# Kernel tuning notes

Measured on AMD Instinct MI355X. Metric: run time of the kernel, lower is better.

## Reference

```python
import jax, jax.numpy as jnp
import numpy as np

B, S, D, H, E = 4, 2048, 1024, 2048, 8
TOP_K = 2


def setup_inputs() -> dict:
    key = jax.random.key(0)
    ks = jax.random.split(key, 6)
    s = 0.02
    x = jax.random.normal(ks[0], (B, S, D), dtype=jnp.float32)
    # torch nn.Linear stores weight as [out_features, in_features]
    W1 = jax.random.normal(ks[1], (E, H, D), dtype=jnp.float32) * s  # dim -> hidden
    W2 = jax.random.normal(ks[2], (E, D, H), dtype=jnp.float32) * s  # hidden -> dim
    W3 = jax.random.normal(ks[3], (E, H, D), dtype=jnp.float32) * s  # dim -> hidden
    gate_w = jax.random.normal(ks[4], (E, D), dtype=jnp.float32) * s
    gate_b = jnp.zeros((E,), dtype=jnp.float32)
    return {"x": x, "W1": W1, "W2": W2, "W3": W3, "gate_w": gate_w, "gate_b": gate_b}


def reference(x, W1, W2, W3, gate_w, gate_b):
    b, s, d = x.shape
    xf = x.reshape(-1, d)                                  # [N, D], N = B*S
    logits = xf @ gate_w.T + gate_b                        # [N, E]
    probs = jax.nn.softmax(logits, axis=-1)
    top2_p, top2_i = jax.lax.top_k(probs, TOP_K)           # [N, 2]
    top2_p = top2_p / jnp.sum(top2_p, axis=-1, keepdims=True)
    out = jnp.zeros_like(xf)
    n_experts = W1.shape[0]
    for e in range(n_experts):  # small fixed expert loop
        # combine weight for tokens routed to expert e (0 if not routed)
        coef = jnp.sum(jnp.where(top2_i == e, top2_p, 0.0), axis=-1)  # [N]
        h = jnp.maximum(xf @ W1[e].T, 0.0) ** 2 * (xf @ W3[e].T)      # relu(x)^2 * x  [N, H]
        out = out + coef[:, None] * (h @ W2[e].T)                     # [N, D]
    return out.reshape(b, s, d)
```

## Files before the change

### kernel.cpp

```cpp
#include <hip/hip_runtime.h>
#include <hip/hip_fp16.h>
#include <math.h>

#define N_TOK 8192
#define D_DIM 1024
#define H_DIM 2048
#define N_EXP 8
#define CAPL  8192
#define MT1   18

typedef _Float16 f16x8 __attribute__((ext_vector_type(8)));
typedef float    f32x4 __attribute__((ext_vector_type(4)));

__device__ __forceinline__ void gload16(const void* g, void* l) {
  __builtin_amdgcn_global_load_lds(
      (const __attribute__((address_space(1))) void*)g,
      (__attribute__((address_space(3))) void*)l, 16, 0, 0);
}

__global__ __launch_bounds__(256) void cvt_f32_f16(const float* __restrict__ s,
                                                   _Float16* __restrict__ d, int n4) {
  int i = blockIdx.x * 256 + threadIdx.x;
  if (i >= n4) return;
  float4 v = ((const float4*)s)[i];
  _Float16 o0 = (_Float16)v.x, o1 = (_Float16)v.y, o2 = (_Float16)v.z, o3 = (_Float16)v.w;
  __attribute__((ext_vector_type(4))) _Float16 o = {o0, o1, o2, o3};
  ((__attribute__((ext_vector_type(4))) _Float16*)d)[i] = o;
}

__global__ __launch_bounds__(256) void pack_w(const float* __restrict__ src,
                                              _Float16* __restrict__ dst,
                                              int R, int K) {
  const int e = blockIdx.z, rt = blockIdx.y, kc = blockIdx.x;
  const int t = threadIdx.x;
  const int r = t >> 1, c = (t & 1) * 16;
  const float* s = src + ((long)e * R + (long)rt * 128 + r) * K + kc * 32 + c;
  const float4 v0 = ((const float4*)s)[0];
  const float4 v1 = ((const float4*)s)[1];
  const float4 v2 = ((const float4*)s)[2];
  const float4 v3 = ((const float4*)s)[3];
  f16x8 o0, o1;
  o0[0]=(_Float16)v0.x; o0[1]=(_Float16)v0.y; o0[2]=(_Float16)v0.z; o0[3]=(_Float16)v0.w;
  o0[4]=(_Float16)v1.x; o0[5]=(_Float16)v1.y; o0[6]=(_Float16)v1.z; o0[7]=(_Float16)v1.w;
  o1[0]=(_Float16)v2.x; o1[1]=(_Float16)v2.y; o1[2]=(_Float16)v2.z; o1[3]=(_Float16)v2.w;
  o1[4]=(_Float16)v3.x; o1[5]=(_Float16)v3.y; o1[6]=(_Float16)v3.z; o1[7]=(_Float16)v3.w;
  _Float16* d = dst + (((long)e * (R >> 7) + rt) * (K >> 5) + kc) * 4096 + t * 16;
  ((f16x8*)d)[0] = o0;
  ((f16x8*)d)[1] = o1;
}

__global__ __launch_bounds__(256) void gate_compute(
    const float* __restrict__ x, const float* __restrict__ gw,
    const float* __restrict__ gb, int* __restrict__ e12,
    float2* __restrict__ pp) {
  __shared__ float sgw[N_EXP * D_DIM];
  for (int i = threadIdx.x; i < N_EXP * D_DIM; i += 256) sgw[i] = gw[i];
  __syncthreads();
  const int w = threadIdx.x >> 6, lane = threadIdx.x & 63;
  const int n = blockIdx.x * 4 + w;
  const float* xp = x + (long)n * D_DIM;
  double acc[N_EXP];
  #pragma unroll
  for (int e = 0; e < N_EXP; e++) acc[e] = 0.0;
  for (int i = 0; i < D_DIM / 64; i++) {
    int d = lane + i * 64;
    double xv = (double)xp[d];
    #pragma unroll
    for (int e = 0; e < N_EXP; e++) acc[e] += xv * (double)sgw[e * D_DIM + d];
  }
  #pragma unroll
  for (int e = 0; e < N_EXP; e++)
    for (int off = 32; off >= 1; off >>= 1)
      acc[e] += __shfl_down(acc[e], off);
  if (lane == 0) {
    double lg[N_EXP];
    #pragma unroll
    for (int e = 0; e < N_EXP; e++) lg[e] = acc[e] + (double)gb[e];
    int i1 = 0;
    for (int e = 1; e < N_EXP; e++) if (lg[e] > lg[i1]) i1 = e;
    int i2 = (i1 == 0) ? 1 : 0;
    for (int e = 0; e < N_EXP; e++) { if (e == i1) continue; if (lg[e] > lg[i2]) i2 = e; }
    double p1 = 1.0 / (1.0 + exp(lg[i2] - lg[i1]));
    double p2 = 1.0 - p1;
    e12[n] = i1 | (i2 << 8);
    pp[n] = make_float2((float)p1, (float)p2);
  }
}

__global__ __launch_bounds__(256) void build_lists(
    const int* __restrict__ e12, const float2* __restrict__ pp,
    int* __restrict__ cnt, int* __restrict__ tokL, float* __restrict__ coefL) {
  const int e = blockIdx.x;
  __shared__ int sbase;
  __shared__ int wsum[4];
  const int w = threadIdx.x >> 6, lane = threadIdx.x & 63;
  if (threadIdx.x == 0) sbase = 0;
  __syncthreads();
  for (int c0 = 0; c0 < N_TOK; c0 += 256) {
    const int n = c0 + threadIdx.x;
    const int v = e12[n];
    const float2 pv = pp[n];
    int slot = -1;
    float p = 0.f;
    if ((v & 255) == e)      { slot = 0; p = pv.x; }
    else if ((v >> 8) == e)  { slot = 1; p = pv.y; }
    const unsigned long long m = __ballot(slot >= 0);
    if (lane == 0) wsum[w] = __popcll(m);
    __syncthreads();
    int wbase = sbase;
    #pragma unroll
    for (int i = 0; i < 4; i++) if (i < w) wbase += wsum[i];
    const int total = wsum[0] + wsum[1] + wsum[2] + wsum[3];
    if (slot >= 0) {
      const int pos = wbase + __popcll(m & ((1ull << lane) - 1ull));
      tokL[e * CAPL + pos] = n * 2 + slot;
      coefL[e * CAPL + pos] = p;
    }
    __syncthreads();
    if (threadIdx.x == 0) sbase += total;
  }
  __syncthreads();
  if (threadIdx.x == 0) cnt[e] = sbase;
}

__global__ __launch_bounds__(384, 2) void ffn_stage1(
    const _Float16* __restrict__ xh, const _Float16* __restrict__ w1p,
    const _Float16* __restrict__ w3p, const int* __restrict__ cnt,
    const int* __restrict__ tokL, _Float16* __restrict__ hbuf) {
  const int lin = blockIdx.x;
  const int xcd = lin & 7;
  const int j   = lin >> 3;
  const int mt  = j % MT1;
  const int gi  = j / MT1;
  const int g   = gi * 8 + xcd;
  const int nt  = g & 15;
  const int e   = g >> 4;
  const int m0 = mt * 128;
  const int c = cnt[e];
  if (m0 >= c) return;

  __shared__ _Float16 Xs[2][4096];
  __shared__ _Float16 W1s[2][4096];
  __shared__ _Float16 W3s[2][4096];
  __shared__ int sEnt[128];

  const int t = threadIdx.x;
  if (t < 128) {
    int idx = m0 + t; if (idx >= c) idx = c - 1;
    sEnt[t] = tokL[e * CAPL + idx];
  }
  __syncthreads();

  if (t >= 256) {
    const int pt = t - 256;
    const int swz = ((pt & 3) ^ ((pt >> 3) & 3)) * 8;
    const _Float16* xsrc[4];
    #pragma unroll
    for (int j2 = 0; j2 < 4; j2++)
      xsrc[j2] = xh + (long)(sEnt[(pt >> 2) + 32 * j2] >> 1) * D_DIM + swz;
    const int po = (pt >> 2) * 32 + swz;
    const _Float16* w1t = w1p + (long)(e * 16 + nt) * 32 * 4096 + po;
    const _Float16* w3t = w3p + (long)(e * 16 + nt) * 32 * 4096 + po;
    const int l0 = pt * 8;

    auto stage = [&](int b, int kc) {
      #pragma unroll
      for (int j2 = 0; j2 < 4; j2++)
        gload16(xsrc[j2] + kc * 32, &Xs[b][l0 + j2 * 1024]);
      #pragma unroll
      for (int j2 = 0; j2 < 4; j2++)
        gload16(w1t + (long)kc * 4096 + j2 * 1024, &W1s[b][l0 + j2 * 1024]);
      #pragma unroll
      for (int j2 = 0; j2 < 4; j2++)
        gload16(w3t + (long)kc * 4096 + j2 * 1024, &W3s[b][l0 + j2 * 1024]);
    };

    stage(0, 0);
    __asm__ volatile("s_waitcnt vmcnt(0)\n\ts_barrier");
    for (int kc = 0; kc < 32; ++kc) {
      if (kc + 1 < 32) stage((kc + 1) & 1, kc + 1);
      __asm__ volatile("s_waitcnt vmcnt(0)\n\ts_barrier");
    }
    return;
  }

  const int w = t >> 6, lane = t & 63;
  const int wm = (w & 1) * 64, wn = (w >> 1) * 64;
  const int q = lane >> 4, lr = lane & 15;
  const int qs = (q ^ ((lr >> 1) & 3)) * 8;

  f32x4 au[4][4], av[4][4];
  const f32x4 zz = {0.f, 0.f, 0.f, 0.f};
  #pragma unroll
  for (int i = 0; i < 4; i++)
    #pragma unroll
    for (int j2 = 0; j2 < 4; j2++) { au[i][j2] = zz; av[i][j2] = zz; }

  __syncthreads();
  for (int kc = 0; kc < 32; ++kc) {
    const int p = kc & 1;
    f16x8 a[4], b1[4], b3[4];
    #pragma unroll
    for (int i = 0; i < 4; i++) {
      a[i]  = *(const f16x8*)(&Xs[p][(wm + i * 16 + lr) * 32 + qs]);
      b1[i] = *(const f16x8*)(&W1s[p][(wn + i * 16 + lr) * 32 + qs]);
      b3[i] = *(const f16x8*)(&W3s[p][(wn + i * 16 + lr) * 32 + qs]);
    }
    #pragma unroll
    for (int mi = 0; mi < 4; mi++)
      #pragma unroll
      for (int ni = 0; ni < 4; ni++) {
        au[mi][ni] = __builtin_amdgcn_mfma_f32_16x16x32_f16(a[mi], b1[ni], au[mi][ni], 0, 0, 0);
        av[mi][ni] = __builtin_amdgcn_mfma_f32_16x16x32_f16(a[mi], b3[ni], av[mi][ni], 0, 0, 0);
      }
    __syncthreads();
  }

  const long tb = ((long)(e * MT1 + mt) * 64 + nt * 4) * 4096;
  #pragma unroll
  for (int mi = 0; mi < 4; mi++) {
    #pragma unroll
    for (int r = 0; r < 4; r++) {
      int ml = wm + mi * 16 + q * 4 + r;
      if (m0 + ml < c) {
        #pragma unroll
        for (int ni = 0; ni < 4; ni++) {
          int colb = wn + ni * 16;
          float u = au[mi][ni][r];
          float rl = u > 0.f ? u : 0.f;
          float hv = rl * rl * av[mi][ni][r];
          hbuf[tb + (long)(colb >> 5) * 4096 + ml * 32 + (colb & 31) + lr] = (_Float16)hv;
        }
      }
    }
  }
}

__global__ __launch_bounds__(384, 3) void ffn_stage2(
    const _Float16* __restrict__ hbuf, const _Float16* __restrict__ w2p,
    const int* __restrict__ cnt, const int* __restrict__ tokL,
    const float* __restrict__ coefL, float* __restrict__ out) {
  const int lin = blockIdx.x;
  const int xcd = lin & 7;
  const int j   = lin >> 3;
  const int mt  = j % MT1;
  const int gi  = j / MT1;
  const int g   = gi * 8 + xcd;
  const int dt  = g & 7;
  const int ezk = g >> 3;
  const int e   = ezk >> 1, ks = ezk & 1;
  const int m0 = mt * 128;
  const int c = cnt[e];
  if (m0 >= c) return;

  __shared__ _Float16 Hs[3][4096];
  __shared__ _Float16 W2s[3][4096];
  __shared__ int sEnt[128];
  __shared__ float sCoef[128];

  const int t = threadIdx.x;
  if (t < 128) {
    int idx = m0 + t; if (idx >= c) idx = c - 1;
    sEnt[t]  = tokL[e * CAPL + idx];
    sCoef[t] = coefL[e * CAPL + idx];
  }
  __syncthreads();

  if (t >= 256) {
    const int pt = t - 256;
    const int swz = ((pt & 3) ^ ((pt >> 3) & 3)) * 8;
    const int po = (pt >> 2) * 32 + swz;
    const _Float16* hA  = hbuf + ((long)(e * MT1 + mt) * 64 + ks * 32) * 4096 + po;
    const _Float16* w2t = w2p  + ((long)(e * 8 + dt) * 64 + ks * 32) * 4096 + po;
    const int l0 = pt * 8;

    auto stage = [&](int b, int kc) {
      #pragma unroll
      for (int j2 = 0; j2 < 4; j2++)
        gload16(hA + (long)kc * 4096 + j2 * 1024, &Hs[b][l0 + j2 * 1024]);
      #pragma unroll
      for (int j2 = 0; j2 < 4; j2++)
        gload16(w2t + (long)kc * 4096 + j2 * 1024, &W2s[b][l0 + j2 * 1024]);
    };

    stage(0, 0); stage(1, 1);
    __asm__ volatile("s_waitcnt vmcnt(8)\n\ts_barrier");
    for (int kc = 0; kc < 32; ++kc) {
      if (kc + 2 < 32) {
        stage((kc + 2) % 3, kc + 2);
        __asm__ volatile("s_waitcnt vmcnt(8)\n\ts_barrier");
      } else {
        __asm__ volatile("s_waitcnt vmcnt(0)\n\ts_barrier");
      }
    }
    return;
  }

  const int w = t >> 6, lane = t & 63;
  const int wm = (w & 1) * 64, wn = (w >> 1) * 64;
  const int q = lane >> 4, lr = lane & 15;
  const int qs = (q ^ ((lr >> 1) & 3)) * 8;

  f32x4 ac[4][4];
  const f32x4 zz = {0.f, 0.f, 0.f, 0.f};
  #pragma unroll
  for (int i = 0; i < 4; i++)
    #pragma unroll
    for (int j2 = 0; j2 < 4; j2++) ac[i][j2] = zz;

  __syncthreads();
  for (int kc = 0; kc < 32; ++kc) {
    const int p = kc % 3;
    f16x8 a[4], b[4];
    #pragma unroll
    for (int i = 0; i < 4; i++) {
      a[i] = *(const f16x8*)(&Hs[p][(wm + i * 16 + lr) * 32 + qs]);
      b[i] = *(const f16x8*)(&W2s[p][(wn + i * 16 + lr) * 32 + qs]);
    }
    #pragma unroll
    for (int mi = 0; mi < 4; mi++)
      #pragma unroll
      for (int ni = 0; ni < 4; ni++)
        ac[mi][ni] = __builtin_amdgcn_mfma_f32_16x16x32_f16(a[mi], b[ni], ac[mi][ni], 0, 0, 0);
    __syncthreads();
  }

  const int n0 = dt * 128;
  #pragma unroll
  for (int mi = 0; mi < 4; mi++) {
    #pragma unroll
    for (int r = 0; r < 4; r++) {
      int ml = wm + mi * 16 + q * 4 + r;
      if (m0 + ml < c) {
        int token = sEnt[ml] >> 1;
        float cf = sCoef[ml];
        float* op = out + (long)token * D_DIM + n0 + wn + lr;
        #pragma unroll
        for (int ni = 0; ni < 4; ni++)
          atomicAdd(op + ni * 16, cf * ac[mi][ni][r]);
      }
    }
  }
}

extern "C" void kernel_launch(void* const* d_in, const int* in_sizes, int n_in,
                              void* d_out, int out_size, void* d_ws, size_t ws_size,
                              hipStream_t stream) {
  (void)in_sizes; (void)n_in; (void)out_size; (void)ws_size;
  const float* x  = (const float*)d_in[0];
  const float* W1 = (const float*)d_in[1];
  const float* W2 = (const float*)d_in[2];
  const float* W3 = (const float*)d_in[3];
  const float* gw = (const float*)d_in[4];
  const float* gb = (const float*)d_in[5];
  float* out = (float*)d_out;

  _Float16* xh  = (_Float16*)d_ws;
  _Float16* w1p = xh  + (size_t)N_TOK * D_DIM;
  _Float16* w3p = w1p + (size_t)N_EXP * H_DIM * D_DIM;
  _Float16* w2p = w3p + (size_t)N_EXP * H_DIM * D_DIM;
  _Float16* hb  = w2p + (size_t)N_EXP * H_DIM * D_DIM;
  int*   cnt   = (int*)(hb + (size_t)N_EXP * MT1 * 64 * 4096);
  int*   tokL  = cnt + 16;
  float* coefL = (float*)(tokL + N_EXP * CAPL);
  int*   e12   = (int*)(coefL + N_EXP * CAPL);
  float2* pp   = (float2*)(e12 + N_TOK);

  hipMemsetAsync(d_out, 0, (size_t)N_TOK * D_DIM * sizeof(float), stream);

  int xn4 = N_TOK * D_DIM / 4;
  cvt_f32_f16<<<(xn4 + 255) / 256, 256, 0, stream>>>(x, xh, xn4);
  pack_w<<<dim3(D_DIM / 32, H_DIM / 128, N_EXP), 256, 0, stream>>>(W1, w1p, H_DIM, D_DIM);
  pack_w<<<dim3(D_DIM / 32, H_DIM / 128, N_EXP), 256, 0, stream>>>(W3, w3p, H_DIM, D_DIM);
  pack_w<<<dim3(H_DIM / 32, D_DIM / 128, N_EXP), 256, 0, stream>>>(W2, w2p, D_DIM, H_DIM);

  gate_compute<<<N_TOK / 4, 256, 0, stream>>>(x, gw, gb, e12, pp);
  build_lists<<<N_EXP, 256, 0, stream>>>(e12, pp, cnt, tokL, coefL);

  ffn_stage1<<<MT1 * 16 * N_EXP, 384, 0, stream>>>(xh, w1p, w3p, cnt, tokL, hb);
  ffn_stage2<<<MT1 * 8 * N_EXP * 2, 384, 0, stream>>>(hb, w2p, cnt, tokL, coefL, out);
}
```

Measured before the change: 687.6 us.

## Drop producer-wave specialization; have compute waves issue their own LDS prefetches

Both FFN GEMM stages previously used 384-thread blocks, with one extra wave group acting only as an async global-to-LDS loader, synchronized with the compute waves through barriers. This removes the producer waves. The 256 compute threads now issue the next k-chunk's global_load_lds themselves at the top of each iteration, with double buffering, and stage 2 drops from triple to double buffering. The goal is to cut the extra waves and their barrier traffic, freeing registers, LDS and wave slots for higher occupancy. The cost is that the compute waves now carry the load issue and wait on the loads at each barrier, with only one stage of prefetch in flight.

```diff
diff --git a/kernel.cpp b/kernel.cpp
--- a/kernel.cpp
+++ b/kernel.cpp
@@ -123,7 +123,7 @@
   if (threadIdx.x == 0) cnt[e] = sbase;
 }
 
-__global__ __launch_bounds__(384, 2) void ffn_stage1(
+__global__ __launch_bounds__(256, 2) void ffn_stage1(
     const _Float16* __restrict__ xh, const _Float16* __restrict__ w1p,
     const _Float16* __restrict__ w3p, const int* __restrict__ cnt,
     const int* __restrict__ tokL, _Float16* __restrict__ hbuf) {
@@ -151,38 +151,22 @@
   }
   __syncthreads();
 
-  if (t >= 256) {
-    const int pt = t - 256;
-    const int swz = ((pt & 3) ^ ((pt >> 3) & 3)) * 8;
-    const _Float16* xsrc[4];
-    #pragma unroll
-    for (int j2 = 0; j2 < 4; j2++)
-      xsrc[j2] = xh + (long)(sEnt[(pt >> 2) + 32 * j2] >> 1) * D_DIM + swz;
-    const int po = (pt >> 2) * 32 + swz;
-    const _Float16* w1t = w1p + (long)(e * 16 + nt) * 32 * 4096 + po;
-    const _Float16* w3t = w3p + (long)(e * 16 + nt) * 32 * 4096 + po;
-    const int l0 = pt * 8;
-
-    auto stage = [&](int b, int kc) {
-      #pragma unroll
-      for (int j2 = 0; j2 < 4; j2++)
-        gload16(xsrc[j2] + kc * 32, &Xs[b][l0 + j2 * 1024]);
-      #pragma unroll
-      for (int j2 = 0; j2 < 4; j2++)
-        gload16(w1t + (long)kc * 4096 + j2 * 1024, &W1s[b][l0 + j2 * 1024]);
-      #pragma unroll
-      for (int j2 = 0; j2 < 4; j2++)
-        gload16(w3t + (long)kc * 4096 + j2 * 1024, &W3s[b][l0 + j2 * 1024]);
-    };
-
-    stage(0, 0);
-    __asm__ volatile("s_waitcnt vmcnt(0)\n\ts_barrier");
-    for (int kc = 0; kc < 32; ++kc) {
-      if (kc + 1 < 32) stage((kc + 1) & 1, kc + 1);
-      __asm__ volatile("s_waitcnt vmcnt(0)\n\ts_barrier");
-    }
-    return;
-  }
+  const int swz = ((t & 3) ^ ((t >> 3) & 3)) * 8;
+  const _Float16* xsrcA = xh + (long)(sEnt[t >> 2] >> 1) * D_DIM + swz;
+  const _Float16* xsrcB = xh + (long)(sEnt[(t >> 2) + 64] >> 1) * D_DIM + swz;
+  const int po = (t >> 2) * 32 + swz;
+  const _Float16* w1t = w1p + (long)(e * 16 + nt) * 32 * 4096 + po;
+  const _Float16* w3t = w3p + (long)(e * 16 + nt) * 32 * 4096 + po;
+  const int l0 = t * 8;
+
+  auto stage = [&](int b, int kc) {
+    gload16(xsrcA + kc * 32, &Xs[b][l0]);
+    gload16(xsrcB + kc * 32, &Xs[b][l0 + 2048]);
+    gload16(w1t + (long)kc * 4096, &W1s[b][l0]);
+    gload16(w1t + (long)kc * 4096 + 2048, &W1s[b][l0 + 2048]);
+    gload16(w3t + (long)kc * 4096, &W3s[b][l0]);
+    gload16(w3t + (long)kc * 4096 + 2048, &W3s[b][l0 + 2048]);
+  };
 
   const int w = t >> 6, lane = t & 63;
   const int wm = (w & 1) * 64, wn = (w >> 1) * 64;
@@ -196,8 +180,10 @@
     #pragma unroll
     for (int j2 = 0; j2 < 4; j2++) { au[i][j2] = zz; av[i][j2] = zz; }
 
+  stage(0, 0);
   __syncthreads();
   for (int kc = 0; kc < 32; ++kc) {
+    if (kc + 1 < 32) stage((kc + 1) & 1, kc + 1);
     const int p = kc & 1;
     f16x8 a[4], b1[4], b3[4];
     #pragma unroll
@@ -236,7 +222,7 @@
   }
 }
 
-__global__ __launch_bounds__(384, 3) void ffn_stage2(
+__global__ __launch_bounds__(256, 3) void ffn_stage2(
     const _Float16* __restrict__ hbuf, const _Float16* __restrict__ w2p,
     const int* __restrict__ cnt, const int* __restrict__ tokL,
     const float* __restrict__ coefL, float* __restrict__ out) {
@@ -253,8 +239,8 @@
   const int c = cnt[e];
   if (m0 >= c) return;
 
-  __shared__ _Float16 Hs[3][4096];
-  __shared__ _Float16 W2s[3][4096];
+  __shared__ _Float16 Hs[2][4096];
+  __shared__ _Float16 W2s[2][4096];
   __shared__ int sEnt[128];
   __shared__ float sCoef[128];
 
@@ -266,35 +252,18 @@
   }
   __syncthreads();
 
-  if (t >= 256) {
-    const int pt = t - 256;
-    const int swz = ((pt & 3) ^ ((pt >> 3) & 3)) * 8;
-    const int po = (pt >> 2) * 32 + swz;
-    const _Float16* hA  = hbuf + ((long)(e * MT1 + mt) * 64 + ks * 32) * 4096 + po;
-    const _Float16* w2t = w2p  + ((long)(e * 8 + dt) * 64 + ks * 32) * 4096 + po;
-    const int l0 = pt * 8;
-
-    auto stage = [&](int b, int kc) {
-      #pragma unroll
-      for (int j2 = 0; j2 < 4; j2++)
-        gload16(hA + (long)kc * 4096 + j2 * 1024, &Hs[b][l0 + j2 * 1024]);
-      #pragma unroll
-      for (int j2 = 0; j2 < 4; j2++)
-        gload16(w2t + (long)kc * 4096 + j2 * 1024, &W2s[b][l0 + j2 * 1024]);
-    };
-
-    stage(0, 0); stage(1, 1);
-    __asm__ volatile("s_waitcnt vmcnt(8)\n\ts_barrier");
-    for (int kc = 0; kc < 32; ++kc) {
-      if (kc + 2 < 32) {
-        stage((kc + 2) % 3, kc + 2);
-        __asm__ volatile("s_waitcnt vmcnt(8)\n\ts_barrier");
-      } else {
-        __asm__ volatile("s_waitcnt vmcnt(0)\n\ts_barrier");
-      }
-    }
-    return;
-  }
+  const int swz = ((t & 3) ^ ((t >> 3) & 3)) * 8;
+  const int po = (t >> 2) * 32 + swz;
+  const _Float16* hA  = hbuf + ((long)(e * MT1 + mt) * 64 + ks * 32) * 4096 + po;
+  const _Float16* w2t = w2p  + ((long)(e * 8 + dt) * 64 + ks * 32) * 4096 + po;
+  const int l0 = t * 8;
+
+  auto stage = [&](int b, int kc) {
+    gload16(hA + (long)kc * 4096, &Hs[b][l0]);
+    gload16(hA + (long)kc * 4096 + 2048, &Hs[b][l0 + 2048]);
+    gload16(w2t + (long)kc * 4096, &W2s[b][l0]);
+    gload16(w2t + (long)kc * 4096 + 2048, &W2s[b][l0 + 2048]);
+  };
 
   const int w = t >> 6, lane = t & 63;
   const int wm = (w & 1) * 64, wn = (w >> 1) * 64;
@@ -308,9 +277,11 @@
     #pragma unroll
     for (int j2 = 0; j2 < 4; j2++) ac[i][j2] = zz;
 
+  stage(0, 0);
   __syncthreads();
   for (int kc = 0; kc < 32; ++kc) {
-    const int p = kc % 3;
+    if (kc + 1 < 32) stage((kc + 1) & 1, kc + 1);
+    const int p = kc & 1;
     f16x8 a[4], b[4];
     #pragma unroll
     for (int i = 0; i < 4; i++) {
@@ -377,6 +348,6 @@
   gate_compute<<<N_TOK / 4, 256, 0, stream>>>(x, gw, gb, e12, pp);
   build_lists<<<N_EXP, 256, 0, stream>>>(e12, pp, cnt, tokL, coefL);
 
-  ffn_stage1<<<MT1 * 16 * N_EXP, 384, 0, stream>>>(xh, w1p, w3p, cnt, tokL, hb);
-  ffn_stage2<<<MT1 * 8 * N_EXP * 2, 384, 0, stream>>>(hb, w2p, cnt, tokL, coefL, out);
-}
+  ffn_stage1<<<MT1 * 16 * N_EXP, 256, 0, stream>>>(xh, w1p, w3p, cnt, tokL, hb);
+  ffn_stage2<<<MT1 * 8 * N_EXP * 2, 256, 0, stream>>>(hb, w2p, cnt, tokL, coefL, out);
+}
```

Measured after the change: 736.3 us. 7.1% more time.
